# Kernel tuning notes

Hardware: AMD Instinct MI355X
Metric: run time of the kernel (lower is better)

## Reference

```python
import jax, jax.numpy as jnp
import numpy as np

IN_DIM = 128
DIM = 32

def setup_inputs() -> dict:
    key = jax.random.key(0)
    ks = jax.random.split(key, 7)
    b, r, L = 1, 128, 256
    m = jax.random.normal(ks[0], (b, r, L, IN_DIM), dtype=jnp.float32)
    ln_w = jnp.ones((IN_DIM,), dtype=jnp.float32)
    ln_b = jnp.zeros((IN_DIM,), dtype=jnp.float32)
    W1 = jax.random.normal(ks[1], (2 * DIM, IN_DIM), dtype=jnp.float32) / np.sqrt(IN_DIM)
    b1 = jax.random.normal(ks[2], (2 * DIM,), dtype=jnp.float32) * 0.01
    W2 = jax.random.normal(ks[3], (IN_DIM, DIM * DIM), dtype=jnp.float32) / np.sqrt(DIM * DIM)
    b2 = jax.random.normal(ks[4], (IN_DIM,), dtype=jnp.float32) * 0.01
    return {"m": m, "ln_w": ln_w, "ln_b": ln_b, "W1": W1, "b1": b1, "W2": W2, "b2": b2}

def reference(m, ln_w, ln_b, W1, b1, W2, b2):
    nrow = m.shape[1]
    # LayerNorm over last dim
    mu = jnp.mean(m, axis=-1, keepdims=True)
    var = jnp.var(m, axis=-1, keepdims=True)
    mn = (m - mu) / jnp.sqrt(var + 1e-5) * ln_w + ln_b
    # projection to a, b (chunk on last dim)
    proj = jnp.einsum('bric,fc->brif', mn, W1) + b1  # [b,r,L,2*DIM]
    a, bb = proj[..., :DIM], proj[..., DIM:]
    # outer-product mean over rows r
    out = jnp.einsum('bric,brjd->bijcd', a, bb) / nrow  # [b,L,L,DIM,DIM]
    B, I, J = out.shape[0], out.shape[1], out.shape[2]
    out = out.reshape(B, I, J, DIM * DIM)
    z = jnp.einsum('bijk,fk->bijf', out, W2) + b2  # [b,L,L,IN_DIM]
    return z
```

## Files before the change

kernel.cpp:

```cpp
#include <hip/hip_runtime.h>
#include <stdint.h>

typedef __attribute__((ext_vector_type(8))) short  short8;
typedef __attribute__((ext_vector_type(4))) float  f32x4;

static __device__ __forceinline__ uint32_t f2bf(float x) {
    union { float f; uint32_t u; } v; v.f = x;
    return (v.u + 0x7FFFu + ((v.u >> 16) & 1u)) >> 16;
}


__global__ __launch_bounds__(256) void prep_weights(
    const float* __restrict__ W2, const float* __restrict__ W1,
    uint16_t* __restrict__ W2f, uint16_t* __restrict__ W1f) {
    int bid = blockIdx.x, t = threadIdx.x;
    if (bid < 512) {
        int idx = bid * 256 + t;
        int f  = idx >> 10;
        int kd = idx & 1023;
        int d = kd >> 5, c = kd & 31;
        int ftile = f >> 4, l16 = f & 15;
        int ks = kd >> 5, kh = (kd >> 3) & 3, e = kd & 7;
        W2f[(size_t)(ftile * 32 + ks) * 512 + (l16 + 16 * kh) * 8 + e] =
            (uint16_t)f2bf(W2[f * 1024 + c * 32 + d]);
    } else {
        int idx = (bid - 512) * 256 + t;
        int f = idx >> 7, c = idx & 127;
        int ftile = f >> 4, l16 = f & 15;
        int ks = c >> 5, kh = (c >> 3) & 3, e = c & 7;
        W1f[(size_t)(ftile * 4 + ks) * 512 + (l16 + 16 * kh) * 8 + e] =
            (uint16_t)f2bf(W1[f * 128 + c]);
    }
}

__global__ __launch_bounds__(256) void ln_proj(
    const float* __restrict__ mI, const float* __restrict__ lnw,
    const float* __restrict__ lnb, const uint16_t* __restrict__ W1f,
    const float* __restrict__ b1,
    uint16_t* __restrict__ At, uint16_t* __restrict__ Bt)
{
    __shared__ __align__(16) uint16_t mns[256 * 8];
    const int t = threadIdx.x;
    const int bid = blockIdx.x;
    const int i0 = (bid * 16) & 255;
    const int r  = bid >> 4;

    {
        int row = t >> 4, cb = t & 15;
        const float* rp = mI + ((size_t)bid * 16 + row) * 128 + cb * 8;
        float4 v0 = *(const float4*)(rp);
        float4 v1 = *(const float4*)(rp + 4);
        float s  = v0.x + v0.y + v0.z + v0.w + v1.x + v1.y + v1.z + v1.w;
        float ss = v0.x*v0.x + v0.y*v0.y + v0.z*v0.z + v0.w*v0.w
                 + v1.x*v1.x + v1.y*v1.y + v1.z*v1.z + v1.w*v1.w;
        #pragma unroll
        for (int off = 8; off > 0; off >>= 1) {
            s  += __shfl_xor(s, off);
            ss += __shfl_xor(ss, off);
        }
        float mean = s * (1.0f / 128.0f);
        float var  = ss * (1.0f / 128.0f) - mean * mean;
        float rstd = rsqrtf(var + 1e-5f);
        float4 wa = *(const float4*)(lnw + cb * 8);
        float4 wb = *(const float4*)(lnw + cb * 8 + 4);
        float4 ba = *(const float4*)(lnb + cb * 8);
        float4 bb = *(const float4*)(lnb + cb * 8 + 4);
        uint16_t y[8];
        y[0] = (uint16_t)f2bf((v0.x - mean) * rstd * wa.x + ba.x);
        y[1] = (uint16_t)f2bf((v0.y - mean) * rstd * wa.y + ba.y);
        y[2] = (uint16_t)f2bf((v0.z - mean) * rstd * wa.z + ba.z);
        y[3] = (uint16_t)f2bf((v0.w - mean) * rstd * wa.w + ba.w);
        y[4] = (uint16_t)f2bf((v1.x - mean) * rstd * wb.x + bb.x);
        y[5] = (uint16_t)f2bf((v1.y - mean) * rstd * wb.y + bb.y);
        y[6] = (uint16_t)f2bf((v1.z - mean) * rstd * wb.z + bb.z);
        y[7] = (uint16_t)f2bf((v1.w - mean) * rstd * wb.w + bb.w);
        int g = cb * 16 + (row ^ (cb & 7));
        *(uint2*)&mns[g * 8]     = *(uint2*)&y[0];
        *(uint2*)&mns[g * 8 + 4] = *(uint2*)&y[4];
    }
    __syncthreads();

    const int w = t >> 6, l = t & 63;
    const int l16 = l & 15, lh = l >> 4;
    f32x4 acc = (f32x4)(0.0f);
    #pragma unroll
    for (int ks = 0; ks < 4; ++ks) {
        int cb = ks * 4 + lh;
        int g  = cb * 16 + (l16 ^ (cb & 7));
        short8 a = *(const short8*)&mns[g * 8];
        short8 b = *(const short8*)(W1f + (size_t)(w * 4 + ks) * 512 + l * 8);
        acc = __builtin_amdgcn_mfma_f32_16x16x32_bf16(a, b, acc, 0, 0, 0);
    }
    float b1v = b1[w * 16 + l16];
    uint16_t* dst = (w < 2) ? At : Bt;
    const float scale = (w < 2) ? (1.0f / 128.0f) : 1.0f;
    const int cch = w & 1;
    const int base2 = (r >> 5) * 512 + (l16 + 16 * ((r >> 3) & 3)) * 8 + (r & 7);
    #pragma unroll
    for (int v = 0; v < 4; ++v) {
        int i = i0 + lh * 4 + v;
        int mtile = i * 2 + cch;
        dst[(size_t)mtile * 2048 + base2] = (uint16_t)f2bf((acc[v] + b1v) * scale);
    }
}

extern __shared__ uint16_t outl[];
__global__ __launch_bounds__(512, 4) void fused_opm(
    const uint16_t* __restrict__ At, const uint16_t* __restrict__ Bt,
    const uint16_t* __restrict__ W2f, const float* __restrict__ b2,
    float* __restrict__ z)
{
    const int t = threadIdx.x;
    const int w = t >> 6, l = t & 63;
    const int l16 = l & 15, lh = l >> 4;
    const int bx = blockIdx.x, by = blockIdx.y;
    const int wm = w >> 1, wn = w & 1;

    f32x4 acc[4][4];
    #pragma unroll
    for (int a = 0; a < 4; ++a)
        #pragma unroll
        for (int b = 0; b < 4; ++b) acc[a][b] = (f32x4)(0.0f);

    const uint16_t* Abase = At + (size_t)(by * 16 + wm * 4) * 4 * 512 + l * 8;
    const uint16_t* Bbase = Bt + (size_t)(bx * 8 + wn * 4) * 4 * 512 + l * 8;
    #pragma unroll
    for (int ks = 0; ks < 4; ++ks) {
        short8 af[4], bf[4];
        #pragma unroll
        for (int mt = 0; mt < 4; ++mt)
            af[mt] = *(const short8*)(Abase + (size_t)(mt * 4 + ks) * 512);
        #pragma unroll
        for (int nt = 0; nt < 4; ++nt)
            bf[nt] = *(const short8*)(Bbase + (size_t)(nt * 4 + ks) * 512);
        #pragma unroll
        for (int mt = 0; mt < 4; ++mt)
            #pragma unroll
            for (int nt = 0; nt < 4; ++nt)
                acc[mt][nt] = __builtin_amdgcn_mfma_f32_16x16x32_bf16(
                    af[mt], bf[nt], acc[mt][nt], 0, 0, 0);
    }

    const uint16_t* Wt = W2f + (size_t)w * 32 * 512 + l * 8;
    short8 wbuf[8];
    #pragma unroll
    for (int q = 0; q < 8; ++q)
        wbuf[q] = *(const short8*)(Wt + (size_t)q * 512);

    #pragma unroll
    for (int mt = 0; mt < 4; ++mt) {
        const int kh = (mt & 1) * 2 + (lh >> 1);
        const int e0 = (lh & 1) * 4;
        #pragma unroll
        for (int nt = 0; nt < 4; ++nt) {
            int p  = wm * 8 + (mt >> 1) * 4 + wn * 2 + (nt >> 1);
            int ks = (nt & 1) * 16 + l16;
            int ptw = p >> 4, l16t = p & 15;
            f32x4 v = acc[mt][nt];
            uint2 pk;
            pk.x = f2bf(v[0]) | (f2bf(v[1]) << 16);
            pk.y = f2bf(v[2]) | (f2bf(v[3]) << 16);
            uint32_t byte = (uint32_t)(ptw * 32 + ks) * 1024u
                          + (uint32_t)(l16t + 16 * kh) * 16u + (uint32_t)e0 * 2u;
            byte ^= (uint32_t)(ks & 7) << 4;
            *(uint2*)((char*)outl + byte) = pk;
        }
    }
    __syncthreads();

    f32x4 zacc[2][2];
    #pragma unroll
    for (int a = 0; a < 2; ++a) { zacc[a][0] = (f32x4)(0.0f); zacc[a][1] = (f32x4)(0.0f); }

    const char* outb = (const char*)outl;
    #define OB0(ksv) ((((uint32_t)(ksv) * 1024u + (uint32_t)l * 16u)) ^ ((uint32_t)((ksv) & 7) << 4))
    #define OB1(ksv) ((((uint32_t)(32 + (ksv)) * 1024u + (uint32_t)l * 16u)) ^ ((uint32_t)((ksv) & 7) << 4))

    short8 o0c = *(const short8*)(outb + OB0(0));
    short8 o1c = *(const short8*)(outb + OB1(0));
    #pragma unroll
    for (int ks = 0; ks < 32; ++ks) {
        short8 cw = wbuf[ks & 7];
        if (ks < 24) wbuf[ks & 7] = *(const short8*)(Wt + (size_t)(ks + 8) * 512);
        short8 o0 = o0c, o1 = o1c;
        if (ks < 31) {
            o0c = *(const short8*)(outb + OB0(ks + 1));
            o1c = *(const short8*)(outb + OB1(ks + 1));
        }
        zacc[0][ks & 1] = __builtin_amdgcn_mfma_f32_16x16x32_bf16(cw, o0, zacc[0][ks & 1], 0, 0, 0);
        zacc[1][ks & 1] = __builtin_amdgcn_mfma_f32_16x16x32_bf16(cw, o1, zacc[1][ks & 1], 0, 0, 0);
    }
    #undef OB0
    #undef OB1

    const int f0 = w * 16 + lh * 4;
    const float4 bv = *(const float4*)(b2 + f0);
    #pragma unroll
    for (int pt = 0; pt < 2; ++pt) {
        int p  = pt * 16 + l16;
        int zi = by * 8 + (p >> 2);
        int zj = bx * 4 + (p & 3);
        float* zrow = z + ((size_t)zi * 256 + zj) * 128;
        float4 zr;
        zr.x = zacc[pt][0][0] + zacc[pt][1][0] + bv.x;
        zr.y = zacc[pt][0][1] + zacc[pt][1][1] + bv.y;
        zr.z = zacc[pt][0][2] + zacc[pt][1][2] + bv.z;
        zr.w = zacc[pt][0][3] + zacc[pt][1][3] + bv.w;
        *(float4*)(zrow + f0) = zr;
    }
}

extern "C" void kernel_launch(void* const* d_in, const int* in_sizes, int n_in,
                              void* d_out, int out_size, void* d_ws, size_t ws_size,
                              hipStream_t stream) {
    const float* m_in = (const float*)d_in[0];
    const float* ln_w = (const float*)d_in[1];
    const float* ln_b = (const float*)d_in[2];
    const float* W1   = (const float*)d_in[3];
    const float* b1   = (const float*)d_in[4];
    const float* W2   = (const float*)d_in[5];
    const float* b2   = (const float*)d_in[6];
    float* z = (float*)d_out;

    uint16_t* At  = (uint16_t*)d_ws;
    uint16_t* Bt  = At + 8192 * 128;
    uint16_t* W2f = Bt + 8192 * 128;
    uint16_t* W1f = W2f + 128 * 1024;

    prep_weights<<<544, 256, 0, stream>>>(W2, W1, W2f, W1f);
    ln_proj<<<2048, 256, 0, stream>>>(m_in, ln_w, ln_b, W1f, b1, At, Bt);
    fused_opm<<<dim3(64, 32), 512, 64 * 1024, stream>>>(At, Bt, W2f, b2, z);
}
```

Baseline: 63.35 us.

## Fold W2 prep into ln_proj, swizzle block order, raise MFMA priority

The W2 bf16 repacking moves into extra blocks of ln_proj so it runs alongside the LayerNorm/projection work, leaving only a small W1 prep kernel. fused_opm switches to a 1D grid with a remapped block index, so consecutively scheduled blocks are spread across XCDs and neighbouring tiles share A/B data in cache. s_setprio is raised around the MFMA loops to favour waves issuing matrix ops. The intent is to cut launch and serialization overhead and improve L2 locality. The risk is that the block remap or the priority hints could hurt scheduling.

```diff
diff --git a/kernel.cpp b/kernel.cpp
--- a/kernel.cpp
+++ b/kernel.cpp
@@ -10,12 +10,27 @@
 }
 
 
-__global__ __launch_bounds__(256) void prep_weights(
-    const float* __restrict__ W2, const float* __restrict__ W1,
-    uint16_t* __restrict__ W2f, uint16_t* __restrict__ W1f) {
-    int bid = blockIdx.x, t = threadIdx.x;
-    if (bid < 512) {
-        int idx = bid * 256 + t;
+__global__ __launch_bounds__(256) void prep_w1(
+    const float* __restrict__ W1, uint16_t* __restrict__ W1f) {
+    int idx = blockIdx.x * 256 + threadIdx.x;
+    int f = idx >> 7, c = idx & 127;
+    int ftile = f >> 4, l16 = f & 15;
+    int ks = c >> 5, kh = (c >> 3) & 3, e = c & 7;
+    W1f[(size_t)(ftile * 4 + ks) * 512 + (l16 + 16 * kh) * 8 + e] =
+        (uint16_t)f2bf(W1[f * 128 + c]);
+}
+
+__global__ __launch_bounds__(256) void ln_proj(
+    const float* __restrict__ mI, const float* __restrict__ lnw,
+    const float* __restrict__ lnb, const uint16_t* __restrict__ W1f,
+    const float* __restrict__ b1, const float* __restrict__ W2,
+    uint16_t* __restrict__ At, uint16_t* __restrict__ Bt,
+    uint16_t* __restrict__ W2f)
+{
+    const int t = threadIdx.x;
+    const int bid = blockIdx.x;
+    if (bid >= 2048) {
+        int idx = (bid - 2048) * 256 + t;
         int f  = idx >> 10;
         int kd = idx & 1023;
         int d = kd >> 5, c = kd & 31;
@@ -23,25 +38,10 @@
         int ks = kd >> 5, kh = (kd >> 3) & 3, e = kd & 7;
         W2f[(size_t)(ftile * 32 + ks) * 512 + (l16 + 16 * kh) * 8 + e] =
             (uint16_t)f2bf(W2[f * 1024 + c * 32 + d]);
-    } else {
-        int idx = (bid - 512) * 256 + t;
-        int f = idx >> 7, c = idx & 127;
-        int ftile = f >> 4, l16 = f & 15;
-        int ks = c >> 5, kh = (c >> 3) & 3, e = c & 7;
-        W1f[(size_t)(ftile * 4 + ks) * 512 + (l16 + 16 * kh) * 8 + e] =
-            (uint16_t)f2bf(W1[f * 128 + c]);
-    }
-}
-
-__global__ __launch_bounds__(256) void ln_proj(
-    const float* __restrict__ mI, const float* __restrict__ lnw,
-    const float* __restrict__ lnb, const uint16_t* __restrict__ W1f,
-    const float* __restrict__ b1,
-    uint16_t* __restrict__ At, uint16_t* __restrict__ Bt)
-{
+        return;
+    }
+
     __shared__ __align__(16) uint16_t mns[256 * 8];
-    const int t = threadIdx.x;
-    const int bid = blockIdx.x;
     const int i0 = (bid * 16) & 255;
     const int r  = bid >> 4;
 
@@ -113,7 +113,9 @@
     const int t = threadIdx.x;
     const int w = t >> 6, l = t & 63;
     const int l16 = l & 15, lh = l >> 4;
-    const int bx = blockIdx.x, by = blockIdx.y;
+    const int id = blockIdx.x;
+    const int lg = ((id & 7) << 8) | (id >> 3);
+    const int bx = lg & 63, by = lg >> 6;
     const int wm = w >> 1, wn = w & 1;
 
     f32x4 acc[4][4];
@@ -124,6 +126,7 @@
 
     const uint16_t* Abase = At + (size_t)(by * 16 + wm * 4) * 4 * 512 + l * 8;
     const uint16_t* Bbase = Bt + (size_t)(bx * 8 + wn * 4) * 4 * 512 + l * 8;
+    __builtin_amdgcn_s_setprio(1);
     #pragma unroll
     for (int ks = 0; ks < 4; ++ks) {
         short8 af[4], bf[4];
@@ -140,6 +143,7 @@
                 acc[mt][nt] = __builtin_amdgcn_mfma_f32_16x16x32_bf16(
                     af[mt], bf[nt], acc[mt][nt], 0, 0, 0);
     }
+    __builtin_amdgcn_s_setprio(0);
 
     const uint16_t* Wt = W2f + (size_t)w * 32 * 512 + l * 8;
     short8 wbuf[8];
@@ -178,6 +182,7 @@
 
     short8 o0c = *(const short8*)(outb + OB0(0));
     short8 o1c = *(const short8*)(outb + OB1(0));
+    __builtin_amdgcn_s_setprio(1);
     #pragma unroll
     for (int ks = 0; ks < 32; ++ks) {
         short8 cw = wbuf[ks & 7];
@@ -190,6 +195,7 @@
         zacc[0][ks & 1] = __builtin_amdgcn_mfma_f32_16x16x32_bf16(cw, o0, zacc[0][ks & 1], 0, 0, 0);
         zacc[1][ks & 1] = __builtin_amdgcn_mfma_f32_16x16x32_bf16(cw, o1, zacc[1][ks & 1], 0, 0, 0);
     }
+    __builtin_amdgcn_s_setprio(0);
     #undef OB0
     #undef OB1
 
@@ -227,7 +233,7 @@
     uint16_t* W2f = Bt + 8192 * 128;
     uint16_t* W1f = W2f + 128 * 1024;
 
-    prep_weights<<<544, 256, 0, stream>>>(W2, W1, W2f, W1f);
-    ln_proj<<<2048, 256, 0, stream>>>(m_in, ln_w, ln_b, W1f, b1, At, Bt);
-    fused_opm<<<dim3(64, 32), 512, 64 * 1024, stream>>>(At, Bt, W2f, b2, z);
-}
+    prep_w1<<<32, 256, 0, stream>>>(W1, W1f);
+    ln_proj<<<2560, 256, 0, stream>>>(m_in, ln_w, ln_b, W1f, b1, W2, At, Bt, W2f);
+    fused_opm<<<2048, 512, 64 * 1024, stream>>>(At, Bt, W2f, b2, z);
+}
```

Measured after the change: 63.49 us. No clear change (+0.2%).
